# Kernel optimization log

Measured on AMD Instinct MI355X. Metric: run time of the kernel, lower is better.

The kernel has to match this reference:

```python
import jax, jax.numpy as jnp
import numpy as np

B, NX, NY, H = 512, 128, 128, 512


def setup_inputs() -> dict:
    key = jax.random.key(0)
    ks = jax.random.split(key, 8)
    s1 = 1.0 / np.sqrt(NX + NY)
    s2 = 1.0 / np.sqrt(H)
    return {
        "x": jax.random.normal(ks[0], (B, NX), dtype=jnp.float32),
        "y": jax.random.normal(ks[1], (B, NY), dtype=jnp.float32),
        "W1": jax.random.normal(ks[2], (H, NX + NY), dtype=jnp.float32) * s1,
        "b1": jax.random.normal(ks[3], (H,), dtype=jnp.float32) * s1,
        "W2": jax.random.normal(ks[4], (H, H), dtype=jnp.float32) * s2,
        "b2": jax.random.normal(ks[5], (H,), dtype=jnp.float32) * s2,
        "W3": jax.random.normal(ks[6], (1, H), dtype=jnp.float32) * s2,
        "b3": jax.random.normal(ks[7], (1,), dtype=jnp.float32) * s2,
    }


def reference(x, y, W1, b1, W2, b2, W3, b3):
    # Torch semantics: pair_input row k = concat(x[k % B], y[k // B]),
    # so scores.view(B,B)[i, j] = mlp(concat(x[j], y[i])).
    Nx = x.shape[1]
    hx = jnp.einsum('jn,hn->jh', x, W1[:, :Nx])          # [B_x, H]
    hy = jnp.einsum('in,hn->ih', y, W1[:, Nx:])          # [B_y, H]
    h1 = jax.nn.relu(hy[:, None, :] + hx[None, :, :] + b1)   # [B_y, B_x, H]
    h2 = jax.nn.relu(jnp.einsum('ijh,gh->ijg', h1, W2) + b2)  # [B_y, B_x, H]
    scores = jnp.einsum('ijh,oh->ijo', h2, W3) + b3          # [B_y, B_x, 1]
    return (scores[..., 0], 0.0)
```

## Files before the change

### kernel.cpp

```cpp
#include <hip/hip_runtime.h>

#define B_ 512
#define H_ 512

typedef short short8 __attribute__((ext_vector_type(8)));
typedef float f32x4 __attribute__((ext_vector_type(4)));

__device__ __forceinline__ unsigned short bf16rne(float f) {
  unsigned u = __float_as_uint(f);
  u += 0x7FFFu + ((u >> 16) & 1u);
  return (unsigned short)(u >> 16);
}

__global__ __launch_bounds__(256) void k_pre(const float* __restrict__ x,
                                             const float* __restrict__ y,
                                             const float* __restrict__ W1,
                                             const float* __restrict__ b1,
                                             const float* __restrict__ W2,
                                             float* __restrict__ hx,
                                             float* __restrict__ hy,
                                             unsigned short* __restrict__ w2p) {
  __shared__ float xs[4][128];
  const int blk = blockIdx.x;
  const int t = threadIdx.x;
  if (blk < 256) {
    const bool isx = blk < 128;
    const int r0 = (isx ? blk : blk - 128) * 4;
    const float* src = (isx ? x : y) + r0 * 128;
    if (t < 128) ((float4*)xs)[t] = ((const float4*)src)[t];
    __syncthreads();
    const int woff = isx ? 0 : 128;
    float* dst = (isx ? hx : hy) + r0 * H_;
#pragma unroll
    for (int hh = 0; hh < 2; ++hh) {
      const int h = t + hh * 256;
      const float4* wr = (const float4*)(W1 + h * 256 + woff);
      float a0 = isx ? b1[h] : 0.f, a1 = a0, a2 = a0, a3 = a0;
#pragma unroll
      for (int n = 0; n < 32; ++n) {
        float4 w = wr[n];
        float4 v0 = ((const float4*)xs[0])[n];
        float4 v1 = ((const float4*)xs[1])[n];
        float4 v2 = ((const float4*)xs[2])[n];
        float4 v3 = ((const float4*)xs[3])[n];
        a0 = fmaf(w.x, v0.x, fmaf(w.y, v0.y, fmaf(w.z, v0.z, fmaf(w.w, v0.w, a0))));
        a1 = fmaf(w.x, v1.x, fmaf(w.y, v1.y, fmaf(w.z, v1.z, fmaf(w.w, v1.w, a1))));
        a2 = fmaf(w.x, v2.x, fmaf(w.y, v2.y, fmaf(w.z, v2.z, fmaf(w.w, v2.w, a2))));
        a3 = fmaf(w.x, v3.x, fmaf(w.y, v3.y, fmaf(w.z, v3.z, fmaf(w.w, v3.w, a3))));
      }
      dst[h] = a0;
      dst[H_ + h] = a1;
      dst[2 * H_ + h] = a2;
      dst[3 * H_ + h] = a3;
    }
  } else {
    int d = (blk - 256) * 256 + t;
    int e = d & 7;
    int g15 = (d >> 3) & 15;
    int ks = (d >> 7) & 3;
    int nf = (d >> 9) & 7;
    int plane = (d >> 12) & 1;
    int c = (d >> 13) & 15;
    int nt = (d >> 17) & 3;
    int g = nt * 128 + nf * 16 + g15;
    int k = c * 32 + ks * 8 + e;
    float v = W2[g * H_ + k];
    unsigned short h = bf16rne(v);
    float r = v - __uint_as_float(((unsigned)h) << 16);
    w2p[d] = plane ? bf16rne(r) : h;
  }
}

__device__ __forceinline__ unsigned chop2(float x0, float x1, float y0,
                                          float y1) {
  float t0 = fmaxf(x0 + y0, 0.f);
  float t1 = fmaxf(x1 + y1, 0.f);
  return __builtin_amdgcn_perm(__float_as_uint(t1), __float_as_uint(t0),
                               0x07060302);
}

union F8 { float4 v4[2]; float f[8]; };
struct FragSet {
  union { unsigned u[4]; short8 s; } a0, a1;
};

#define BUILD_PAIR(NXT, p_)                                                   \
  {                                                                           \
    if ((p_) < 4)                                                             \
      NXT.a0.u[(p_)] = chop2(X.f[2 * (p_)], X.f[2 * (p_) + 1],                \
                             Y0.f[2 * (p_)], Y0.f[2 * (p_) + 1]);             \
    else                                                                      \
      NXT.a1.u[(p_) - 4] =                                                    \
          chop2(X.f[2 * ((p_) - 4)], X.f[2 * ((p_) - 4) + 1],                 \
                Y1.f[2 * ((p_) - 4)], Y1.f[2 * ((p_) - 4) + 1]);              \
  }

#define CHUNK_STEP(c_, buf_, CUR, NXT)                                        \
  {                                                                           \
    if ((c_) < 15) STAGE((c_) + 1, (buf_) ^ 1);                               \
    const int ko_ = ((c_) + 1) * 32;                                          \
    X.v4[0] = *(const float4*)(hxp + ko_);                                    \
    X.v4[1] = *(const float4*)(hxp + ko_ + 4);                                \
    Y0.v4[0] = *(const float4*)(hyp0 + ko_);                                  \
    Y0.v4[1] = *(const float4*)(hyp0 + ko_ + 4);                              \
    Y1.v4[0] = *(const float4*)(hyp1 + ko_);                                  \
    Y1.v4[1] = *(const float4*)(hyp1 + ko_ + 4);                              \
    const unsigned short* bb_ = (buf_) ? bbr1 : bbr0;                         \
    _Pragma("unroll") for (int nf = 0; nf < 8; ++nf) {                        \
      short8 Bh = *(const short8*)(bb_ + nf * 512);                           \
      short8 Bl = *(const short8*)(bb_ + 4096 + nf * 512);                    \
      __builtin_amdgcn_s_setprio(1);                                          \
      f32x4 a0 = acc[0][nf];                                                  \
      a0 = __builtin_amdgcn_mfma_f32_16x16x32_bf16(CUR.a0.s, Bl, a0, 0, 0, 0);\
      a0 = __builtin_amdgcn_mfma_f32_16x16x32_bf16(CUR.a0.s, Bh, a0, 0, 0, 0);\
      acc[0][nf] = a0;                                                        \
      f32x4 a1 = acc[1][nf];                                                  \
      a1 = __builtin_amdgcn_mfma_f32_16x16x32_bf16(CUR.a1.s, Bl, a1, 0, 0, 0);\
      a1 = __builtin_amdgcn_mfma_f32_16x16x32_bf16(CUR.a1.s, Bh, a1, 0, 0, 0);\
      acc[1][nf] = a1;                                                        \
      __builtin_amdgcn_s_setprio(0);                                          \
      if (nf >= 4) {                                                          \
        BUILD_PAIR(NXT, 2 * (nf - 4));                                        \
        BUILD_PAIR(NXT, 2 * (nf - 4) + 1);                                    \
      }                                                                       \
    }                                                                         \
    __syncthreads();                                                          \
  }

__global__ __launch_bounds__(256, 4) void k_main(
    const float* __restrict__ hx, const float* __restrict__ hy,
    const unsigned short* __restrict__ w2p,
    const float* __restrict__ b2, const float* __restrict__ w3,
    const float* __restrict__ b3, float* __restrict__ out) {
  __shared__ alignas(16) unsigned short Bs[2][8192];

  const int tid = threadIdx.x;
  const int lane = tid & 63;
  const int wid = tid >> 6;

  const int bid = blockIdx.x;
  const int ntile = bid & 3;
  const int mtile = bid >> 2;
  const int ibase = (mtile >> 5) << 3;
  const int jbase = (mtile & 31) << 4;
  const int l15 = lane & 15;
  const int kslot = (lane >> 4) << 3;

  const float* hxp = hx + (jbase + l15) * H_ + kslot;
  const float* hyp0 = hy + (ibase + wid * 2 + 0) * H_ + kslot;
  const float* hyp1 = hy + (ibase + wid * 2 + 1) * H_ + kslot;

  const unsigned short* gstage = w2p + ntile * 131072 + wid * 2048 + lane * 8;
  unsigned short* lds_dst0 = &Bs[0][wid * 2048];
  unsigned short* lds_dst1 = &Bs[1][wid * 2048];
  const unsigned short* bbr0 = &Bs[0][0] + lane * 8;
  const unsigned short* bbr1 = &Bs[1][0] + lane * 8;

  auto STAGE = [&](int c, int buf) {
    const unsigned short* g = gstage + c * 8192;
    unsigned short* l = buf ? lds_dst1 : lds_dst0;
#pragma unroll
    for (int q = 0; q < 4; ++q) {
      __builtin_amdgcn_global_load_lds(
          (const __attribute__((address_space(1))) unsigned int*)(g + q * 512),
          (__attribute__((address_space(3))) unsigned int*)(l + q * 512),
          16, 0, 0);
    }
  };

  f32x4 acc[2][8] = {};
  FragSet F, G;
  F8 X, Y0, Y1;

  STAGE(0, 0);
  X.v4[0] = *(const float4*)(hxp);
  X.v4[1] = *(const float4*)(hxp + 4);
  Y0.v4[0] = *(const float4*)(hyp0);
  Y0.v4[1] = *(const float4*)(hyp0 + 4);
  Y1.v4[0] = *(const float4*)(hyp1);
  Y1.v4[1] = *(const float4*)(hyp1 + 4);
#pragma unroll
  for (int p = 0; p < 8; ++p) BUILD_PAIR(F, p);
  __syncthreads();

  for (int cc = 0; cc < 8; ++cc) {
    CHUNK_STEP(2 * cc, 0, F, G);
    CHUNK_STEP(2 * cc + 1, 1, G, F);
  }

  const int gbase = ntile << 7;
  float b2v[8], w3v[8];
#pragma unroll
  for (int nf = 0; nf < 8; ++nf) {
    int g = gbase + nf * 16 + l15;
    b2v[nf] = b2[g];
    w3v[nf] = w3[g];
  }
  const float b3v = (ntile == 0) ? b3[0] : 0.f;
#pragma unroll
  for (int mf = 0; mf < 2; ++mf) {
#pragma unroll
    for (int r = 0; r < 4; ++r) {
      float s = 0.f;
#pragma unroll
      for (int nf = 0; nf < 8; ++nf) {
        float h2 = fmaxf(acc[mf][nf][r] + b2v[nf], 0.f);
        s = fmaf(w3v[nf], h2, s);
      }
      s += __shfl_xor(s, 1);
      s += __shfl_xor(s, 2);
      s += __shfl_xor(s, 4);
      s += __shfl_xor(s, 8);
      if (l15 == 0) {
        int jl = ((lane >> 4) << 2) + r;
        int il = wid * 2 + mf;
        atomicAdd(out + (ibase + il) * B_ + jbase + jl, s + b3v);
      }
    }
  }
}

extern "C" void kernel_launch(void* const* d_in, const int* in_sizes, int n_in,
                              void* d_out, int out_size, void* d_ws, size_t ws_size,
                              hipStream_t stream) {
  const float* x  = (const float*)d_in[0];
  const float* y  = (const float*)d_in[1];
  const float* W1 = (const float*)d_in[2];
  const float* b1 = (const float*)d_in[3];
  const float* W2 = (const float*)d_in[4];
  const float* b2 = (const float*)d_in[5];
  const float* W3 = (const float*)d_in[6];
  const float* b3 = (const float*)d_in[7];
  float* out = (float*)d_out;

  char* ws = (char*)d_ws;
  float* hx = (float*)ws;
  float* hy = (float*)(ws + (1u << 20));
  unsigned short* w2p = (unsigned short*)(ws + (2u << 20));

  hipMemsetAsync(d_out, 0, (size_t)out_size * sizeof(float), stream);
  k_pre<<<2304, 256, 0, stream>>>(x, y, W1, b1, W2, hx, hy, w2p);
  k_main<<<8192, 256, 0, stream>>>(hx, hy, w2p, b2, W3, b3, out);
}
```

Baseline: 339.6 us.

## Restructure main kernel into independent per-wave tiles loading W2 directly from global

Measured after the change: 759.7 us. +123.7%, slower.

```diff
diff --git a/kernel.cpp b/kernel.cpp
--- a/kernel.cpp
+++ b/kernel.cpp
@@ -58,11 +58,11 @@
     int e = d & 7;
     int g15 = (d >> 3) & 15;
     int ks = (d >> 7) & 3;
-    int nf = (d >> 9) & 7;
-    int plane = (d >> 12) & 1;
-    int c = (d >> 13) & 15;
-    int nt = (d >> 17) & 3;
-    int g = nt * 128 + nf * 16 + g15;
+    int nf = (d >> 9) & 3;
+    int plane = (d >> 11) & 1;
+    int c = (d >> 12) & 15;
+    int gt = d >> 16;
+    int g = gt * 64 + nf * 16 + g15;
     int k = c * 32 + ks * 8 + e;
     float v = W2[g * H_ + k];
     unsigned short h = bf16rne(v);
@@ -79,131 +79,98 @@
                                0x07060302);
 }
 
-union F8 { float4 v4[2]; float f[8]; };
-struct FragSet {
-  union { unsigned u[4]; short8 s; } a0, a1;
-};
-
-#define BUILD_PAIR(NXT, p_)                                                   \
-  {                                                                           \
-    if ((p_) < 4)                                                             \
-      NXT.a0.u[(p_)] = chop2(X.f[2 * (p_)], X.f[2 * (p_) + 1],                \
-                             Y0.f[2 * (p_)], Y0.f[2 * (p_) + 1]);             \
-    else                                                                      \
-      NXT.a1.u[(p_) - 4] =                                                    \
-          chop2(X.f[2 * ((p_) - 4)], X.f[2 * ((p_) - 4) + 1],                 \
-                Y1.f[2 * ((p_) - 4)], Y1.f[2 * ((p_) - 4) + 1]);              \
-  }
-
-#define CHUNK_STEP(c_, buf_, CUR, NXT)                                        \
-  {                                                                           \
-    if ((c_) < 15) STAGE((c_) + 1, (buf_) ^ 1);                               \
-    const int ko_ = ((c_) + 1) * 32;                                          \
-    X.v4[0] = *(const float4*)(hxp + ko_);                                    \
-    X.v4[1] = *(const float4*)(hxp + ko_ + 4);                                \
-    Y0.v4[0] = *(const float4*)(hyp0 + ko_);                                  \
-    Y0.v4[1] = *(const float4*)(hyp0 + ko_ + 4);                              \
-    Y1.v4[0] = *(const float4*)(hyp1 + ko_);                                  \
-    Y1.v4[1] = *(const float4*)(hyp1 + ko_ + 4);                              \
-    const unsigned short* bb_ = (buf_) ? bbr1 : bbr0;                         \
-    _Pragma("unroll") for (int nf = 0; nf < 8; ++nf) {                        \
-      short8 Bh = *(const short8*)(bb_ + nf * 512);                           \
-      short8 Bl = *(const short8*)(bb_ + 4096 + nf * 512);                    \
-      __builtin_amdgcn_s_setprio(1);                                          \
-      f32x4 a0 = acc[0][nf];                                                  \
-      a0 = __builtin_amdgcn_mfma_f32_16x16x32_bf16(CUR.a0.s, Bl, a0, 0, 0, 0);\
-      a0 = __builtin_amdgcn_mfma_f32_16x16x32_bf16(CUR.a0.s, Bh, a0, 0, 0, 0);\
-      acc[0][nf] = a0;                                                        \
-      f32x4 a1 = acc[1][nf];                                                  \
-      a1 = __builtin_amdgcn_mfma_f32_16x16x32_bf16(CUR.a1.s, Bl, a1, 0, 0, 0);\
-      a1 = __builtin_amdgcn_mfma_f32_16x16x32_bf16(CUR.a1.s, Bh, a1, 0, 0, 0);\
-      acc[1][nf] = a1;                                                        \
-      __builtin_amdgcn_s_setprio(0);                                          \
-      if (nf >= 4) {                                                          \
-        BUILD_PAIR(NXT, 2 * (nf - 4));                                        \
-        BUILD_PAIR(NXT, 2 * (nf - 4) + 1);                                    \
-      }                                                                       \
-    }                                                                         \
-    __syncthreads();                                                          \
-  }
-
-__global__ __launch_bounds__(256, 4) void k_main(
+__global__ __launch_bounds__(256, 3) void k_main(
     const float* __restrict__ hx, const float* __restrict__ hy,
     const unsigned short* __restrict__ w2p,
     const float* __restrict__ b2, const float* __restrict__ w3,
     const float* __restrict__ b3, float* __restrict__ out) {
-  __shared__ alignas(16) unsigned short Bs[2][8192];
-
   const int tid = threadIdx.x;
   const int lane = tid & 63;
   const int wid = tid >> 6;
 
-  const int bid = blockIdx.x;
-  const int ntile = bid & 3;
-  const int mtile = bid >> 2;
-  const int ibase = (mtile >> 5) << 3;
-  const int jbase = (mtile & 31) << 4;
+  const int wv = blockIdx.x * 4 + wid;
+  const int pt = wv >> 3;
+  const int gt = wv & 7;
+  const int ibase = (pt >> 5) << 2;
+  const int jbase = (pt & 31) << 4;
   const int l15 = lane & 15;
   const int kslot = (lane >> 4) << 3;
 
   const float* hxp = hx + (jbase + l15) * H_ + kslot;
-  const float* hyp0 = hy + (ibase + wid * 2 + 0) * H_ + kslot;
-  const float* hyp1 = hy + (ibase + wid * 2 + 1) * H_ + kslot;
-
-  const unsigned short* gstage = w2p + ntile * 131072 + wid * 2048 + lane * 8;
-  unsigned short* lds_dst0 = &Bs[0][wid * 2048];
-  unsigned short* lds_dst1 = &Bs[1][wid * 2048];
-  const unsigned short* bbr0 = &Bs[0][0] + lane * 8;
-  const unsigned short* bbr1 = &Bs[1][0] + lane * 8;
-
-  auto STAGE = [&](int c, int buf) {
-    const unsigned short* g = gstage + c * 8192;
-    unsigned short* l = buf ? lds_dst1 : lds_dst0;
-#pragma unroll
-    for (int q = 0; q < 4; ++q) {
-      __builtin_amdgcn_global_load_lds(
-          (const __attribute__((address_space(1))) unsigned int*)(g + q * 512),
-          (__attribute__((address_space(3))) unsigned int*)(l + q * 512),
-          16, 0, 0);
-    }
-  };
-
-  f32x4 acc[2][8] = {};
-  FragSet F, G;
-  F8 X, Y0, Y1;
-
-  STAGE(0, 0);
-  X.v4[0] = *(const float4*)(hxp);
-  X.v4[1] = *(const float4*)(hxp + 4);
-  Y0.v4[0] = *(const float4*)(hyp0);
-  Y0.v4[1] = *(const float4*)(hyp0 + 4);
-  Y1.v4[0] = *(const float4*)(hyp1);
-  Y1.v4[1] = *(const float4*)(hyp1 + 4);
-#pragma unroll
-  for (int p = 0; p < 8; ++p) BUILD_PAIR(F, p);
-  __syncthreads();
-
-  for (int cc = 0; cc < 8; ++cc) {
-    CHUNK_STEP(2 * cc, 0, F, G);
-    CHUNK_STEP(2 * cc + 1, 1, G, F);
-  }
-
-  const int gbase = ntile << 7;
-  float b2v[8], w3v[8];
-#pragma unroll
-  for (int nf = 0; nf < 8; ++nf) {
+  const float* hyp = hy + ibase * H_ + kslot;
+
+  const unsigned short* bp0 = w2p + gt * 65536 + lane * 8;
+  const unsigned short* bp1 = bp0 + 2048;
+
+  f32x4 acc[4][4] = {};
+
+  float4 X0 = *(const float4*)(hxp);
+  float4 X1 = *(const float4*)(hxp + 4);
+  float4 Ya[4], Yb[4];
+#pragma unroll
+  for (int mf = 0; mf < 4; ++mf) {
+    Ya[mf] = *(const float4*)(hyp + mf * H_);
+    Yb[mf] = *(const float4*)(hyp + mf * H_ + 4);
+  }
+
+#pragma unroll 1
+  for (int c = 0; c < 16; ++c) {
+    const unsigned short* b0 = bp0 + c * 4096;
+    const unsigned short* b1 = bp1 + c * 4096;
+    short8 Bh[4], Bl[4];
+#pragma unroll
+    for (int nf = 0; nf < 4; ++nf) {
+      Bh[nf] = *(const short8*)(b0 + nf * 512);
+      Bl[nf] = *(const short8*)(b1 + nf * 512);
+    }
+    union { unsigned u[4]; short8 s; } A[4];
+#pragma unroll
+    for (int mf = 0; mf < 4; ++mf) {
+      A[mf].u[0] = chop2(X0.x, X0.y, Ya[mf].x, Ya[mf].y);
+      A[mf].u[1] = chop2(X0.z, X0.w, Ya[mf].z, Ya[mf].w);
+      A[mf].u[2] = chop2(X1.x, X1.y, Yb[mf].x, Yb[mf].y);
+      A[mf].u[3] = chop2(X1.z, X1.w, Yb[mf].z, Yb[mf].w);
+    }
+    if (c < 15) {
+      const int ko = (c + 1) * 32;
+      X0 = *(const float4*)(hxp + ko);
+      X1 = *(const float4*)(hxp + ko + 4);
+#pragma unroll
+      for (int mf = 0; mf < 4; ++mf) {
+        Ya[mf] = *(const float4*)(hyp + mf * H_ + ko);
+        Yb[mf] = *(const float4*)(hyp + mf * H_ + ko + 4);
+      }
+    }
+#pragma unroll
+    for (int nf = 0; nf < 4; ++nf) {
+      __builtin_amdgcn_s_setprio(1);
+#pragma unroll
+      for (int mf = 0; mf < 4; ++mf) {
+        f32x4 a = acc[mf][nf];
+        a = __builtin_amdgcn_mfma_f32_16x16x32_bf16(A[mf].s, Bl[nf], a, 0, 0, 0);
+        a = __builtin_amdgcn_mfma_f32_16x16x32_bf16(A[mf].s, Bh[nf], a, 0, 0, 0);
+        acc[mf][nf] = a;
+      }
+      __builtin_amdgcn_s_setprio(0);
+    }
+  }
+
+  const int gbase = gt << 6;
+  float b2v[4], w3v[4];
+#pragma unroll
+  for (int nf = 0; nf < 4; ++nf) {
     int g = gbase + nf * 16 + l15;
     b2v[nf] = b2[g];
     w3v[nf] = w3[g];
   }
-  const float b3v = (ntile == 0) ? b3[0] : 0.f;
-#pragma unroll
-  for (int mf = 0; mf < 2; ++mf) {
+  const float b3v = (gt == 0) ? b3[0] : 0.f;
+#pragma unroll
+  for (int mf = 0; mf < 4; ++mf) {
 #pragma unroll
     for (int r = 0; r < 4; ++r) {
       float s = 0.f;
 #pragma unroll
-      for (int nf = 0; nf < 8; ++nf) {
+      for (int nf = 0; nf < 4; ++nf) {
         float h2 = fmaxf(acc[mf][nf][r] + b2v[nf], 0.f);
         s = fmaf(w3v[nf], h2, s);
       }
@@ -213,8 +180,7 @@
       s += __shfl_xor(s, 8);
       if (l15 == 0) {
         int jl = ((lane >> 4) << 2) + r;
-        int il = wid * 2 + mf;
-        atomicAdd(out + (ibase + il) * B_ + jbase + jl, s + b3v);
+        atomicAdd(out + (ibase + mf) * B_ + jbase + jl, s + b3v);
       }
     }
   }
```

## Double per-wave M tile to four y-rows to reuse staged W2 tiles

Applied to the files above, without the earlier changes.

New measurement: 302.6 us. 1.12x faster.

```diff
diff --git a/kernel.cpp b/kernel.cpp
--- a/kernel.cpp
+++ b/kernel.cpp
@@ -79,55 +79,44 @@
                                0x07060302);
 }
 
-union F8 { float4 v4[2]; float f[8]; };
-struct FragSet {
-  union { unsigned u[4]; short8 s; } a0, a1;
-};
-
-#define BUILD_PAIR(NXT, p_)                                                   \
+union Frag { unsigned u[4]; short8 s; };
+
+#define BUILD_FRAG(NXT, m_)                                                   \
   {                                                                           \
-    if ((p_) < 4)                                                             \
-      NXT.a0.u[(p_)] = chop2(X.f[2 * (p_)], X.f[2 * (p_) + 1],                \
-                             Y0.f[2 * (p_)], Y0.f[2 * (p_) + 1]);             \
-    else                                                                      \
-      NXT.a1.u[(p_) - 4] =                                                    \
-          chop2(X.f[2 * ((p_) - 4)], X.f[2 * ((p_) - 4) + 1],                 \
-                Y1.f[2 * ((p_) - 4)], Y1.f[2 * ((p_) - 4) + 1]);              \
+    NXT[m_].u[0] = chop2(X0.x, X0.y, Ya[m_].x, Ya[m_].y);                     \
+    NXT[m_].u[1] = chop2(X0.z, X0.w, Ya[m_].z, Ya[m_].w);                     \
+    NXT[m_].u[2] = chop2(X1.x, X1.y, Yb[m_].x, Yb[m_].y);                     \
+    NXT[m_].u[3] = chop2(X1.z, X1.w, Yb[m_].z, Yb[m_].w);                     \
   }
 
 #define CHUNK_STEP(c_, buf_, CUR, NXT)                                        \
   {                                                                           \
     if ((c_) < 15) STAGE((c_) + 1, (buf_) ^ 1);                               \
     const int ko_ = ((c_) + 1) * 32;                                          \
-    X.v4[0] = *(const float4*)(hxp + ko_);                                    \
-    X.v4[1] = *(const float4*)(hxp + ko_ + 4);                                \
-    Y0.v4[0] = *(const float4*)(hyp0 + ko_);                                  \
-    Y0.v4[1] = *(const float4*)(hyp0 + ko_ + 4);                              \
-    Y1.v4[0] = *(const float4*)(hyp1 + ko_);                                  \
-    Y1.v4[1] = *(const float4*)(hyp1 + ko_ + 4);                              \
+    X0 = *(const float4*)(hxp + ko_);                                         \
+    X1 = *(const float4*)(hxp + ko_ + 4);                                     \
+    _Pragma("unroll") for (int m = 0; m < 4; ++m) {                           \
+      Ya[m] = *(const float4*)(hyp + m * H_ + ko_);                           \
+      Yb[m] = *(const float4*)(hyp + m * H_ + ko_ + 4);                       \
+    }                                                                         \
     const unsigned short* bb_ = (buf_) ? bbr1 : bbr0;                         \
     _Pragma("unroll") for (int nf = 0; nf < 8; ++nf) {                        \
       short8 Bh = *(const short8*)(bb_ + nf * 512);                           \
       short8 Bl = *(const short8*)(bb_ + 4096 + nf * 512);                    \
       __builtin_amdgcn_s_setprio(1);                                          \
-      f32x4 a0 = acc[0][nf];                                                  \
-      a0 = __builtin_amdgcn_mfma_f32_16x16x32_bf16(CUR.a0.s, Bl, a0, 0, 0, 0);\
-      a0 = __builtin_amdgcn_mfma_f32_16x16x32_bf16(CUR.a0.s, Bh, a0, 0, 0, 0);\
-      acc[0][nf] = a0;                                                        \
-      f32x4 a1 = acc[1][nf];                                                  \
-      a1 = __builtin_amdgcn_mfma_f32_16x16x32_bf16(CUR.a1.s, Bl, a1, 0, 0, 0);\
-      a1 = __builtin_amdgcn_mfma_f32_16x16x32_bf16(CUR.a1.s, Bh, a1, 0, 0, 0);\
-      acc[1][nf] = a1;                                                        \
+      _Pragma("unroll") for (int m = 0; m < 4; ++m) {                         \
+        f32x4 a = acc[m][nf];                                                 \
+        a = __builtin_amdgcn_mfma_f32_16x16x32_bf16(CUR[m].s, Bl, a, 0, 0, 0);\
+        a = __builtin_amdgcn_mfma_f32_16x16x32_bf16(CUR[m].s, Bh, a, 0, 0, 0);\
+        acc[m][nf] = a;                                                       \
+      }                                                                       \
       __builtin_amdgcn_s_setprio(0);                                          \
-      if (nf >= 4) {                                                          \
-        BUILD_PAIR(NXT, 2 * (nf - 4));                                        \
-        BUILD_PAIR(NXT, 2 * (nf - 4) + 1);                                    \
-      }                                                                       \
+      if ((nf) >= 4) BUILD_FRAG(NXT, (nf) - 4);                               \
     }                                                                         \
     __syncthreads();                                                          \
   }
 
-__global__ __launch_bounds__(256, 4) void k_main(
+__global__ __launch_bounds__(256, 2) void k_main(
     const float* __restrict__ hx, const float* __restrict__ hy,
     const unsigned short* __restrict__ w2p,
     const float* __restrict__ b2, const float* __restrict__ w3,
@@ -141,14 +130,13 @@
   const int bid = blockIdx.x;
   const int ntile = bid & 3;
   const int mtile = bid >> 2;
-  const int ibase = (mtile >> 5) << 3;
+  const int ibase = (mtile >> 5) << 4;
   const int jbase = (mtile & 31) << 4;
   const int l15 = lane & 15;
   const int kslot = (lane >> 4) << 3;
 
   const float* hxp = hx + (jbase + l15) * H_ + kslot;
-  const float* hyp0 = hy + (ibase + wid * 2 + 0) * H_ + kslot;
-  const float* hyp1 = hy + (ibase + wid * 2 + 1) * H_ + kslot;
+  const float* hyp = hy + (ibase + wid * 4) * H_ + kslot;
 
   const unsigned short* gstage = w2p + ntile * 131072 + wid * 2048 + lane * 8;
   unsigned short* lds_dst0 = &Bs[0][wid * 2048];
@@ -168,19 +156,20 @@
     }
   };
 
-  f32x4 acc[2][8] = {};
-  FragSet F, G;
-  F8 X, Y0, Y1;
+  f32x4 acc[4][8] = {};
+  Frag F[4], G[4];
+  float4 X0, X1, Ya[4], Yb[4];
 
   STAGE(0, 0);
-  X.v4[0] = *(const float4*)(hxp);
-  X.v4[1] = *(const float4*)(hxp + 4);
-  Y0.v4[0] = *(const float4*)(hyp0);
-  Y0.v4[1] = *(const float4*)(hyp0 + 4);
-  Y1.v4[0] = *(const float4*)(hyp1);
-  Y1.v4[1] = *(const float4*)(hyp1 + 4);
-#pragma unroll
-  for (int p = 0; p < 8; ++p) BUILD_PAIR(F, p);
+  X0 = *(const float4*)(hxp);
+  X1 = *(const float4*)(hxp + 4);
+#pragma unroll
+  for (int m = 0; m < 4; ++m) {
+    Ya[m] = *(const float4*)(hyp + m * H_);
+    Yb[m] = *(const float4*)(hyp + m * H_ + 4);
+  }
+#pragma unroll
+  for (int m = 0; m < 4; ++m) BUILD_FRAG(F, m);
   __syncthreads();
 
   for (int cc = 0; cc < 8; ++cc) {
@@ -198,7 +187,7 @@
   }
   const float b3v = (ntile == 0) ? b3[0] : 0.f;
 #pragma unroll
-  for (int mf = 0; mf < 2; ++mf) {
+  for (int mf = 0; mf < 4; ++mf) {
 #pragma unroll
     for (int r = 0; r < 4; ++r) {
       float s = 0.f;
@@ -213,7 +202,7 @@
       s += __shfl_xor(s, 8);
       if (l15 == 0) {
         int jl = ((lane >> 4) << 2) + r;
-        int il = wid * 2 + mf;
+        int il = wid * 4 + mf;
         atomicAdd(out + (ibase + il) * B_ + jbase + jl, s + b3v);
       }
     }
@@ -240,5 +229,5 @@
 
   hipMemsetAsync(d_out, 0, (size_t)out_size * sizeof(float), stream);
   k_pre<<<2304, 256, 0, stream>>>(x, y, W1, b1, W2, hx, hy, w2p);
-  k_main<<<8192, 256, 0, stream>>>(hx, hy, w2p, b2, W3, b3, out);
-}
+  k_main<<<4096, 256, 0, stream>>>(hx, hy, w2p, b2, W3, b3, out);
+}
```
